# Performance work log

Measured on AMD Instinct MI355X. Metric: run time of the kernel, lower is better.

## Reference

```python
import jax, jax.numpy as jnp
import numpy as np

NUM_EMBEDDINGS = 8192
EMBEDDING_DIM = 256
COMMITMENT_COST = 0.25


def setup_inputs() -> dict:
    key = jax.random.key(0)
    k1, k2 = jax.random.split(key)
    x = jax.random.normal(k1, (8, 4096, EMBEDDING_DIM), dtype=jnp.float32)
    # torch init: uniform(-1/K, 1/K)
    codebook = jax.random.uniform(
        k2, (NUM_EMBEDDINGS, EMBEDDING_DIM), dtype=jnp.float32,
        minval=-1.0 / NUM_EMBEDDINGS, maxval=1.0 / NUM_EMBEDDINGS)
    return {"x": x, "codebook": codebook}


def reference(x, codebook):
    D = codebook.shape[1]
    K = codebook.shape[0]
    flat_x = x.reshape(-1, D)                      # [N, D]
    distances = (jnp.sum(flat_x * flat_x, axis=1, keepdims=True)
                 + jnp.sum(codebook * codebook, axis=1)
                 - 2.0 * jnp.matmul(flat_x, codebook.T))
    encoding_indices = jnp.argmin(distances, axis=1)  # [N]
    # direct gather instead of one-hot matmul (same math)
    quantized = codebook[encoding_indices].reshape(x.shape)

    sg = jax.lax.stop_gradient
    e_latent_loss = jnp.mean((sg(quantized) - x) ** 2)
    q_latent_loss = jnp.mean((quantized - sg(x)) ** 2)
    loss = q_latent_loss + COMMITMENT_COST * e_latent_loss

    quantized_st = x + sg(quantized - x)

    # avg one-hot probs via counts
    counts = jnp.bincount(encoding_indices, length=K)
    avg_probs = counts.astype(x.dtype) / encoding_indices.shape[0]
    perplexity = jnp.exp(-jnp.sum(avg_probs * jnp.log(avg_probs + 1e-10)))
    return quantized_st, loss, perplexity
```

## Files before the change

### kernel.cpp

```cpp
#include <hip/hip_runtime.h>
#include <cfloat>
#include <math.h>

#define NUM_EMB 8192
#define DIM 256
#define NROWS 32768
#define NSPLIT 4
#define CHUNKS 16

typedef float f32x4 __attribute__((ext_vector_type(4)));
typedef int   i32x4 __attribute__((ext_vector_type(4)));
typedef int   i32x8 __attribute__((ext_vector_type(8)));

#define GL2LDS(g, l) __builtin_amdgcn_global_load_lds( \
    (const __attribute__((address_space(1))) void*)(g), \
    (__attribute__((address_space(3))) void*)(l), 16, 0, 0)

__global__ __launch_bounds__(256) void vq_prep(const float* __restrict__ x,
                                               unsigned char* __restrict__ xq,
                                               const float* __restrict__ cb,
                                               unsigned char* __restrict__ cbq,
                                               float* __restrict__ cbn,
                                               unsigned int* __restrict__ counts) {
    int b = blockIdx.x;
    if (b < 4096) {
        int i = b * 256 + threadIdx.x;
        float4 v0 = ((const float4*)x)[2 * i];
        float4 v1 = ((const float4*)x)[2 * i + 1];
        int p0 = __builtin_amdgcn_cvt_pk_fp8_f32(v0.x, v0.y, 0, false);
        p0     = __builtin_amdgcn_cvt_pk_fp8_f32(v0.z, v0.w, p0, true);
        int p1 = __builtin_amdgcn_cvt_pk_fp8_f32(v1.x, v1.y, 0, false);
        p1     = __builtin_amdgcn_cvt_pk_fp8_f32(v1.z, v1.w, p1, true);
        ((int2*)xq)[i] = make_int2(p0, p1);
    } else if (b < 6144) {
        int row  = (b - 4096) * 4 + (threadIdx.x >> 6);
        int lane = threadIdx.x & 63;
        float4 v = ((const float4*)(cb + (size_t)row * DIM))[lane];
        int p = __builtin_amdgcn_cvt_pk_fp8_f32(v.x * 8192.f, v.y * 8192.f, 0, false);
        p     = __builtin_amdgcn_cvt_pk_fp8_f32(v.z * 8192.f, v.w * 8192.f, p, true);
        ((int*)cbq)[row * 64 + lane] = p;
        float s = v.x * v.x + v.y * v.y + v.z * v.z + v.w * v.w;
        #pragma unroll
        for (int off = 32; off > 0; off >>= 1) s += __shfl_down(s, off, 64);
        if (lane == 0) cbn[row] = 8192.f * s + 512.f;
    } else {
        counts[(b - 6144) * 256 + threadIdx.x] = 0u;
    }
}

__global__ __launch_bounds__(256) void vq_argmin_mfma(
        const unsigned char* __restrict__ xq,
        const unsigned char* __restrict__ cbq,
        const float* __restrict__ cbn,
        unsigned long long* __restrict__ partial) {
    __shared__ __align__(16) unsigned char As[2][128 * 128];
    __shared__ __align__(16) unsigned char Bs[128 * 128];
    __shared__ unsigned long long redk[2][128];

    const int tid = threadIdx.x;
    const int lane = tid & 63;
    const int w = tid >> 6;
    const int wm = w >> 1, wn = w & 1;
    const int l15 = lane & 15, q = lane >> 4;
    const int ns = blockIdx.x & (NSPLIT - 1);
    const int by = blockIdx.x / NSPLIT;
    const int m0 = by * 128;
    const int nbase = ns * (NUM_EMB / NSPLIT);

    const int sub = lane >> 3;
    const int sl  = lane & 7;

    #pragma unroll
    for (int kc = 0; kc < 2; kc++)
        #pragma unroll
        for (int t = 0; t < 4; t++) {
            int seg = t * 4 + w;
            int row = seg * 8 + sub;
            int blk = sl ^ (row & 7);
            GL2LDS((const char*)xq + (size_t)(m0 + row) * 256 + kc * 128 + blk * 16,
                   (char*)As[kc] + seg * 1024);
        }

    unsigned int colb[4];
    #pragma unroll
    for (int j = 0; j < 4; j++) colb[j] = (unsigned)(wn * 64 + j * 16 + l15);

    unsigned int runk[4][4];
    unsigned int runcP[4];
    #pragma unroll
    for (int i = 0; i < 4; i++) {
        runcP[i] = 0u;
        #pragma unroll
        for (int r = 0; r < 4; r++) runk[i][r] = 0xFFFFFFFFu;
    }

    #pragma unroll 1
    for (int ch = 0; ch < CHUNKS; ch++) {
        const int n0c = nbase + ch * 128;
        float bnj[4];
        #pragma unroll
        for (int j = 0; j < 4; j++) bnj[j] = cbn[n0c + (int)colb[j]];

        f32x4 acc[4][4];
        #pragma unroll
        for (int i = 0; i < 4; i++)
            #pragma unroll
            for (int j = 0; j < 4; j++) acc[i][j] = (f32x4)0.f;

        #pragma unroll
        for (int kc = 0; kc < 2; kc++) {
            __syncthreads();
            #pragma unroll
            for (int t = 0; t < 4; t++) {
                int seg = t * 4 + w;
                int row = seg * 8 + sub;
                int blk = sl ^ (row & 7);
                GL2LDS((const char*)cbq + (size_t)(n0c + row) * 256 + kc * 128 + blk * 16,
                       (char*)Bs + seg * 1024);
            }
            __syncthreads();

            i32x8 bfr[4];
            #pragma unroll
            for (int j = 0; j < 4; j++) {
                int row = wn * 64 + j * 16 + l15;
                int s0 = ((2 * q) ^ (row & 7)) * 16;
                int s1 = ((2 * q + 1) ^ (row & 7)) * 16;
                i32x4 lo = *(const i32x4*)(Bs + row * 128 + s0);
                i32x4 hi = *(const i32x4*)(Bs + row * 128 + s1);
                bfr[j] = __builtin_shufflevector(lo, hi, 0, 1, 2, 3, 4, 5, 6, 7);
            }
            #pragma unroll
            for (int i = 0; i < 4; i++) {
                int row = wm * 64 + i * 16 + l15;
                int s0 = ((2 * q) ^ (row & 7)) * 16;
                int s1 = ((2 * q + 1) ^ (row & 7)) * 16;
                i32x4 lo = *(const i32x4*)(As[kc] + row * 128 + s0);
                i32x4 hi = *(const i32x4*)(As[kc] + row * 128 + s1);
                i32x8 afr = __builtin_shufflevector(lo, hi, 0, 1, 2, 3, 4, 5, 6, 7);
                #pragma unroll
                for (int j = 0; j < 4; j++)
                    acc[i][j] = __builtin_amdgcn_mfma_scale_f32_16x16x128_f8f6f4(
                        afr, bfr[j], acc[i][j], 0, 0,
                        0, 127, 0, 127);
            }
        }

        #pragma unroll
        for (int i = 0; i < 4; i++) {
            #pragma unroll
            for (int r = 0; r < 4; r++) {
                unsigned int k0 = (__float_as_uint(fmaf(-2.f, acc[i][0][r], bnj[0])) & 0xFFFFFF80u) | colb[0];
                unsigned int k1 = (__float_as_uint(fmaf(-2.f, acc[i][1][r], bnj[1])) & 0xFFFFFF80u) | colb[1];
                unsigned int k2 = (__float_as_uint(fmaf(-2.f, acc[i][2][r], bnj[2])) & 0xFFFFFF80u) | colb[2];
                unsigned int k3 = (__float_as_uint(fmaf(-2.f, acc[i][3][r], bnj[3])) & 0xFFFFFF80u) | colb[3];
                unsigned int km = min(min(k0, k1), min(k2, k3));
                bool u = km < runk[i][r];
                unsigned int nb = (runcP[i] & ~(0xFFu << (8 * r))) | ((unsigned)ch << (8 * r));
                runk[i][r] = u ? km : runk[i][r];
                runcP[i]   = u ? nb : runcP[i];
            }
        }
    }

    #pragma unroll
    for (int i = 0; i < 4; i++) {
        #pragma unroll
        for (int r = 0; r < 4; r++) {
            unsigned int rk = runk[i][r];
            unsigned int chv = (runcP[i] >> (8 * r)) & 0xFFu;
            unsigned int gcol = (unsigned)nbase + chv * 128u + (rk & 127u);
            unsigned long long key =
                ((unsigned long long)(rk & 0xFFFFFF80u) << 32) | gcol;
            #pragma unroll
            for (int off = 8; off >= 1; off >>= 1) {
                unsigned long long o = __shfl_xor(key, off, 16);
                if (o < key) key = o;
            }
            if (l15 == 0) redk[wn][wm * 64 + i * 16 + q * 4 + r] = key;
        }
    }
    __syncthreads();
    if (tid < 128) {
        unsigned long long k0 = redk[0][tid], k1 = redk[1][tid];
        partial[(size_t)ns * NROWS + m0 + tid] = k0 < k1 ? k0 : k1;
    }
}

__global__ __launch_bounds__(256) void vq_out(const float* __restrict__ x,
                                              const float* __restrict__ cb,
                                              const unsigned long long* __restrict__ partial,
                                              float* __restrict__ out,
                                              unsigned int* __restrict__ counts,
                                              double* __restrict__ loss_part) {
    __shared__ float wred[4];
    int wv   = threadIdx.x >> 6;
    int row  = blockIdx.x * 4 + wv;
    int lane = threadIdx.x & 63;
    unsigned long long k = 0xFFFFFFFFFFFFFFFFull;
    #pragma unroll
    for (int t = 0; t < NSPLIT; t++) {
        unsigned long long v = partial[(size_t)t * NROWS + row];
        if (v < k) k = v;
    }
    int id = (int)(unsigned int)(k & 0xffffffffu);
    float4 qv = ((const float4*)(cb + (size_t)id * DIM))[lane];
    float4 xv = ((const float4*)(x + (size_t)row * DIM))[lane];
    float dx = qv.x - xv.x, dy = qv.y - xv.y, dz = qv.z - xv.z, dw = qv.w - xv.w;
    float4 o;
    o.x = xv.x + dx; o.y = xv.y + dy; o.z = xv.z + dz; o.w = xv.w + dw;
    ((float4*)(out + (size_t)row * DIM))[lane] = o;
    float s = dx * dx + dy * dy + dz * dz + dw * dw;
    #pragma unroll
    for (int o2 = 32; o2 > 0; o2 >>= 1) s += __shfl_down(s, o2, 64);
    if (lane == 0) {
        wred[wv] = s;
        atomicAdd(&counts[id], 1u);
    }
    __syncthreads();
    if (threadIdx.x == 0) {
        loss_part[blockIdx.x] =
            (double)wred[0] + (double)wred[1] + (double)wred[2] + (double)wred[3];
    }
}

__global__ __launch_bounds__(256) void vq_fin(const unsigned int* __restrict__ counts,
                                              const double* __restrict__ loss_part,
                                              float* __restrict__ out_tail) {
    __shared__ double sh[256];
    __shared__ double sl[256];
    int tid = threadIdx.x;
    double h = 0.0;
    for (int k = tid; k < NUM_EMB; k += 256) {
        float p = (float)counts[k] / 32768.0f;
        h += (double)p * log((double)p + 1e-10);
    }
    double ls = 0.0;
    for (int b = tid; b < NROWS / 4; b += 256) ls += loss_part[b];
    sh[tid] = h;
    sl[tid] = ls;
    __syncthreads();
    for (int o = 128; o > 0; o >>= 1) {
        if (tid < o) { sh[tid] += sh[tid + o]; sl[tid] += sl[tid + o]; }
        __syncthreads();
    }
    if (tid == 0) {
        double mean = sl[0] / (double)((size_t)NROWS * DIM);
        out_tail[0] = (float)(1.25 * mean);
        out_tail[1] = (float)exp(-sh[0]);
    }
}

extern "C" void kernel_launch(void* const* d_in, const int* in_sizes, int n_in,
                              void* d_out, int out_size, void* d_ws, size_t ws_size,
                              hipStream_t stream) {
    const float* x  = (const float*)d_in[0];
    const float* cb = (const float*)d_in[1];
    char* ws = (char*)d_ws;
    unsigned int* counts   = (unsigned int*)(ws + 256);
    float* cbn             = (float*)(ws + 33024);
    unsigned char* xq      = (unsigned char*)(ws + 65792);
    unsigned char* cbq     = (unsigned char*)(ws + 65792 + 8388608);
    unsigned long long* pp = (unsigned long long*)(ws + 65792 + 8388608 + 2097152);
    double* loss_part      = (double*)(ws + 65792 + 8388608 + 2097152 + 16777216);
    float* out = (float*)d_out;

    vq_prep       <<<6176, 256, 0, stream>>>(x, xq, cb, cbq, cbn, counts);
    vq_argmin_mfma<<<256 * NSPLIT, 256, 0, stream>>>(xq, cbq, cbn, pp);
    vq_out        <<<8192, 256, 0, stream>>>(x, cb, pp, out, counts, loss_part);
    vq_fin        <<<1, 256, 0, stream>>>(counts, loss_part, out + (size_t)NROWS * DIM);
}
```

Before: 216.5 us.

## Pack chunk index into argmin key and fuse finalize into output kernel

The argmin epilogue now packs the full 11-bit column (chunk and column) into the low bits of the distance key. This replaces the separate per-chunk byte-packed chunk tracker and the select logic with a single min per row. The trade-off is 4 more mantissa bits dropped from the distance, so near-ties resolve more coarsely. The separate single-block finalize kernel is removed: the last vq_out block, detected with an atomic counter reset in vq_prep, computes the loss and perplexity, saving one launch at the cost of a fence and an atomic per block.

Result: slower. 466.1 us (+115.3%).

```diff
diff --git a/kernel.cpp b/kernel.cpp
--- a/kernel.cpp
+++ b/kernel.cpp
@@ -21,7 +21,8 @@
                                                const float* __restrict__ cb,
                                                unsigned char* __restrict__ cbq,
                                                float* __restrict__ cbn,
-                                               unsigned int* __restrict__ counts) {
+                                               unsigned int* __restrict__ counts,
+                                               unsigned int* __restrict__ ctr) {
     int b = blockIdx.x;
     if (b < 4096) {
         int i = b * 256 + threadIdx.x;
@@ -45,6 +46,7 @@
         if (lane == 0) cbn[row] = 8192.f * s + 512.f;
     } else {
         counts[(b - 6144) * 256 + threadIdx.x] = 0u;
+        if (b == 6144 && threadIdx.x == 0) *ctr = 0u;
     }
 }
 
@@ -86,20 +88,22 @@
     for (int j = 0; j < 4; j++) colb[j] = (unsigned)(wn * 64 + j * 16 + l15);
 
     unsigned int runk[4][4];
-    unsigned int runcP[4];
-    #pragma unroll
-    for (int i = 0; i < 4; i++) {
-        runcP[i] = 0u;
+    #pragma unroll
+    for (int i = 0; i < 4; i++)
         #pragma unroll
         for (int r = 0; r < 4; r++) runk[i][r] = 0xFFFFFFFFu;
-    }
 
     #pragma unroll 1
     for (int ch = 0; ch < CHUNKS; ch++) {
         const int n0c = nbase + ch * 128;
+        const unsigned int chb = (unsigned)ch << 7;
+        unsigned int cj[4];
         float bnj[4];
         #pragma unroll
-        for (int j = 0; j < 4; j++) bnj[j] = cbn[n0c + (int)colb[j]];
+        for (int j = 0; j < 4; j++) {
+            cj[j] = chb | colb[j];
+            bnj[j] = cbn[n0c + (int)colb[j]];
+        }
 
         f32x4 acc[4][4];
         #pragma unroll
@@ -150,15 +154,11 @@
         for (int i = 0; i < 4; i++) {
             #pragma unroll
             for (int r = 0; r < 4; r++) {
-                unsigned int k0 = (__float_as_uint(fmaf(-2.f, acc[i][0][r], bnj[0])) & 0xFFFFFF80u) | colb[0];
-                unsigned int k1 = (__float_as_uint(fmaf(-2.f, acc[i][1][r], bnj[1])) & 0xFFFFFF80u) | colb[1];
-                unsigned int k2 = (__float_as_uint(fmaf(-2.f, acc[i][2][r], bnj[2])) & 0xFFFFFF80u) | colb[2];
-                unsigned int k3 = (__float_as_uint(fmaf(-2.f, acc[i][3][r], bnj[3])) & 0xFFFFFF80u) | colb[3];
-                unsigned int km = min(min(k0, k1), min(k2, k3));
-                bool u = km < runk[i][r];
-                unsigned int nb = (runcP[i] & ~(0xFFu << (8 * r))) | ((unsigned)ch << (8 * r));
-                runk[i][r] = u ? km : runk[i][r];
-                runcP[i]   = u ? nb : runcP[i];
+                unsigned int k0 = (__float_as_uint(fmaf(-2.f, acc[i][0][r], bnj[0])) & 0xFFFFF800u) | cj[0];
+                unsigned int k1 = (__float_as_uint(fmaf(-2.f, acc[i][1][r], bnj[1])) & 0xFFFFF800u) | cj[1];
+                unsigned int k2 = (__float_as_uint(fmaf(-2.f, acc[i][2][r], bnj[2])) & 0xFFFFF800u) | cj[2];
+                unsigned int k3 = (__float_as_uint(fmaf(-2.f, acc[i][3][r], bnj[3])) & 0xFFFFF800u) | cj[3];
+                runk[i][r] = min(runk[i][r], min(min(k0, k1), min(k2, k3)));
             }
         }
     }
@@ -168,10 +168,9 @@
         #pragma unroll
         for (int r = 0; r < 4; r++) {
             unsigned int rk = runk[i][r];
-            unsigned int chv = (runcP[i] >> (8 * r)) & 0xFFu;
-            unsigned int gcol = (unsigned)nbase + chv * 128u + (rk & 127u);
+            unsigned int gcol = (unsigned)nbase + (rk & 0x7FFu);
             unsigned long long key =
-                ((unsigned long long)(rk & 0xFFFFFF80u) << 32) | gcol;
+                ((unsigned long long)(rk & 0xFFFFF800u) << 32) | gcol;
             #pragma unroll
             for (int off = 8; off >= 1; off >>= 1) {
                 unsigned long long o = __shfl_xor(key, off, 16);
@@ -192,8 +191,11 @@
                                               const unsigned long long* __restrict__ partial,
                                               float* __restrict__ out,
                                               unsigned int* __restrict__ counts,
-                                              double* __restrict__ loss_part) {
+                                              double* __restrict__ loss_part,
+                                              unsigned int* __restrict__ ctr,
+                                              float* __restrict__ out_tail) {
     __shared__ float wred[4];
+    __shared__ bool lastf;
     int wv   = threadIdx.x >> 6;
     int row  = blockIdx.x * 4 + wv;
     int lane = threadIdx.x & 63;
@@ -221,33 +223,34 @@
     if (threadIdx.x == 0) {
         loss_part[blockIdx.x] =
             (double)wred[0] + (double)wred[1] + (double)wred[2] + (double)wred[3];
-    }
-}
-
-__global__ __launch_bounds__(256) void vq_fin(const unsigned int* __restrict__ counts,
-                                              const double* __restrict__ loss_part,
-                                              float* __restrict__ out_tail) {
-    __shared__ double sh[256];
-    __shared__ double sl[256];
-    int tid = threadIdx.x;
-    double h = 0.0;
-    for (int k = tid; k < NUM_EMB; k += 256) {
-        float p = (float)counts[k] / 32768.0f;
-        h += (double)p * log((double)p + 1e-10);
-    }
-    double ls = 0.0;
-    for (int b = tid; b < NROWS / 4; b += 256) ls += loss_part[b];
-    sh[tid] = h;
-    sl[tid] = ls;
+        __threadfence();
+        lastf = (atomicAdd(ctr, 1u) == gridDim.x - 1);
+    }
     __syncthreads();
-    for (int o = 128; o > 0; o >>= 1) {
-        if (tid < o) { sh[tid] += sh[tid + o]; sl[tid] += sl[tid + o]; }
+    if (lastf) {
+        __threadfence();
+        __shared__ double sh[256];
+        __shared__ double sl2[256];
+        int tid = threadIdx.x;
+        double h = 0.0;
+        for (int c = tid; c < NUM_EMB; c += 256) {
+            float p = (float)counts[c] / 32768.0f;
+            h += (double)p * log((double)p + 1e-10);
+        }
+        double ls = 0.0;
+        for (int b = tid; b < NROWS / 4; b += 256) ls += loss_part[b];
+        sh[tid] = h;
+        sl2[tid] = ls;
         __syncthreads();
-    }
-    if (tid == 0) {
-        double mean = sl[0] / (double)((size_t)NROWS * DIM);
-        out_tail[0] = (float)(1.25 * mean);
-        out_tail[1] = (float)exp(-sh[0]);
+        for (int o2 = 128; o2 > 0; o2 >>= 1) {
+            if (tid < o2) { sh[tid] += sh[tid + o2]; sl2[tid] += sl2[tid + o2]; }
+            __syncthreads();
+        }
+        if (tid == 0) {
+            double mean = sl2[0] / (double)((size_t)NROWS * DIM);
+            out_tail[0] = (float)(1.25 * mean);
+            out_tail[1] = (float)exp(-sh[0]);
+        }
     }
 }
 
@@ -257,6 +260,7 @@
     const float* x  = (const float*)d_in[0];
     const float* cb = (const float*)d_in[1];
     char* ws = (char*)d_ws;
+    unsigned int* ctr      = (unsigned int*)ws;
     unsigned int* counts   = (unsigned int*)(ws + 256);
     float* cbn             = (float*)(ws + 33024);
     unsigned char* xq      = (unsigned char*)(ws + 65792);
@@ -265,8 +269,8 @@
     double* loss_part      = (double*)(ws + 65792 + 8388608 + 2097152 + 16777216);
     float* out = (float*)d_out;
 
-    vq_prep       <<<6176, 256, 0, stream>>>(x, xq, cb, cbq, cbn, counts);
+    vq_prep       <<<6176, 256, 0, stream>>>(x, xq, cb, cbq, cbn, counts, ctr);
     vq_argmin_mfma<<<256 * NSPLIT, 256, 0, stream>>>(xq, cbq, cbn, pp);
-    vq_out        <<<8192, 256, 0, stream>>>(x, cb, pp, out, counts, loss_part);
-    vq_fin        <<<1, 256, 0, stream>>>(counts, loss_part, out + (size_t)NROWS * DIM);
-}
+    vq_out        <<<8192, 256, 0, stream>>>(x, cb, pp, out, counts, loss_part, ctr,
+                                             out + (size_t)NROWS * DIM);
+}
```
